# Performance work log

Hardware: AMD Instinct MI355X
Metric: run time of the kernel (lower is better)

The kernel has to match this reference:

```python
import jax, jax.numpy as jnp
import numpy as np

B, L, D, H = 2, 2048, 2048, 16
HD = D // H  # head_dim = 128
EPS = 1e-5


def setup_inputs() -> dict:
    key = jax.random.key(0)
    ks = jax.random.split(key, 5)
    return {
        "x": jax.random.normal(ks[0], (B, L, D), dtype=jnp.float32),
        "Wq": jax.random.normal(ks[1], (D, D), dtype=jnp.float32) * (D ** -0.5),
        "Wk": jax.random.normal(ks[2], (D, D), dtype=jnp.float32) * (D ** -0.5),
        "Wv": jax.random.normal(ks[3], (D, D), dtype=jnp.float32) * (D ** -0.5),
        "gamma_logit": jax.random.normal(ks[4], (H,), dtype=jnp.float32),
        "gn_weight": jnp.ones((D,), dtype=jnp.float32),
        "gn_bias": jnp.zeros((D,), dtype=jnp.float32),
    }


def reference(x, Wq, Wk, Wv, gamma_logit, gn_weight, gn_bias):
    scale = HD ** -0.5
    # projections (torch Linear: y = x @ W.T)
    Q = jnp.einsum('bld,ed->ble', x, Wq).reshape(B, L, H, HD).transpose(0, 2, 1, 3)
    K = jnp.einsum('bld,ed->ble', x, Wk).reshape(B, L, H, HD).transpose(0, 2, 1, 3)
    V = jnp.einsum('bld,ed->ble', x, Wv).reshape(B, L, H, HD).transpose(0, 2, 1, 3)
    # causal exponential decay matrix D[h,i,j] = gamma_h^(i-j), lower-triangular
    pos = jnp.arange(L)
    dist = jnp.abs(pos[None, :] - pos[:, None]).astype(jnp.float32)  # [L,L]
    gamma = jax.nn.sigmoid(gamma_logit)  # [H]
    Dmat = jnp.tril(gamma[:, None, None] ** dist[None, :, :])  # [H,L,L]
    # decayed linear attention (no softmax)
    attn = jnp.einsum('bhid,bhjd->bhij', Q, K) * scale * Dmat[None]
    out = jnp.einsum('bhij,bhje->bhie', attn, V)  # [B,H,L,HD]
    out = out.transpose(0, 2, 1, 3)  # [B,L,H,HD]
    # GroupNorm: channels=D, groups=H, spatial=L -> normalize per (b,h) over (L,HD)
    mean = out.mean(axis=(1, 3), keepdims=True)
    var = out.var(axis=(1, 3), keepdims=True)
    y = (out - mean) * jax.lax.rsqrt(var + EPS)
    y = y * gn_weight.reshape(1, 1, H, HD) + gn_bias.reshape(1, 1, H, HD)
    return y.reshape(B, L, D)
```

## Files before the change

kernel.cpp:

```cpp
#include <hip/hip_runtime.h>
#include <hip/hip_bf16.h>
#include <math.h>

#define B_  2
#define L_  2048
#define D_  2048
#define H_  16
#define HD_ 128
#define EPS_ 1e-5f

typedef __attribute__((ext_vector_type(8)))  short short8;
typedef __attribute__((ext_vector_type(4)))  float f32x4;
typedef __attribute__((ext_vector_type(16))) float f32x16;

static __device__ inline unsigned short bfb(float x) {
    __hip_bfloat16 h = __float2bfloat16(x);
    unsigned short s;
    __builtin_memcpy(&s, &h, 2);
    return s;
}
static __device__ inline unsigned pk2(float a, float b) {
    return (unsigned)bfb(a) | ((unsigned)bfb(b) << 16);
}

static __device__ __forceinline__ void gld_lds16(const void* g, void* l) {
    __builtin_amdgcn_global_load_lds(
        (const __attribute__((address_space(1))) unsigned int*)g,
        (__attribute__((address_space(3))) unsigned int*)l,
        16, 0, 0);
}

#define XN4 2097152
#define WN4 1048576
#define TOT4 (XN4 + 3 * WN4)

__global__ __launch_bounds__(256) void cast4_kernel(
    const float* __restrict__ x,  const float* __restrict__ Wq,
    const float* __restrict__ Wk, const float* __restrict__ Wv,
    __hip_bfloat16* __restrict__ dst)
{
    int i = blockIdx.x * 256 + threadIdx.x;
    const int st = gridDim.x * 256;
    for (; i < TOT4; i += st) {
        const float* s;
        int off;
        if (i < XN4)                { s = x;  off = i; }
        else if (i < XN4 + WN4)     { s = Wq; off = i - XN4; }
        else if (i < XN4 + 2 * WN4) { s = Wk; off = i - XN4 - WN4; }
        else                        { s = Wv; off = i - XN4 - 2 * WN4; }
        float4 v = ((const float4*)s)[off];
        uint2 r;
        r.x = pk2(v.x, v.y);
        r.y = pk2(v.z, v.w);
        ((uint2*)dst)[i] = r;
    }
}

__global__ __launch_bounds__(256) void proj_bf16(
    const __hip_bfloat16* __restrict__ X,
    const __hip_bfloat16* __restrict__ Wqb, const __hip_bfloat16* __restrict__ Wkb,
    const __hip_bfloat16* __restrict__ Wvb,
    __hip_bfloat16* __restrict__ Qo, __hip_bfloat16* __restrict__ Ko,
    __hip_bfloat16* __restrict__ Vt)
{
    const __hip_bfloat16* W = (blockIdx.z == 0) ? Wqb : (blockIdx.z == 1 ? Wkb : Wvb);
    __hip_bfloat16*       O = (blockIdx.z == 0) ? Qo  : (blockIdx.z == 1 ? Ko  : Vt);

    __shared__ __align__(16) char Al[128 * 64 * 2];
    __shared__ __align__(16) char Bl[128 * 64 * 2];

    const int t  = threadIdx.x;
    const int w  = t >> 6, l = t & 63;
    const int li = l & 15, hi4 = l >> 4;
    const int wr = w >> 1, wcn = w & 1;
    const int m0 = blockIdx.y * 128;
    const int n0 = blockIdx.x * 128;

    const int srow = l >> 3;
    const int scol = ((l & 7) ^ (l >> 3)) * 8;

    f32x4 acc[4][4];
    #pragma unroll
    for (int i = 0; i < 4; ++i)
        #pragma unroll
        for (int j = 0; j < 4; ++j)
            #pragma unroll
            for (int r = 0; r < 4; ++r) acc[i][j][r] = 0.f;

    for (int k0 = 0; k0 < D_; k0 += 64) {
        if (k0) __syncthreads();
        #pragma unroll
        for (int c = 0; c < 4; ++c) {
            const int chunk = w * 4 + c;
            const int row   = chunk * 8 + srow;
            gld_lds16(X + (size_t)(m0 + row) * D_ + k0 + scol, Al + chunk * 1024);
            gld_lds16(W + (size_t)(n0 + row) * D_ + k0 + scol, Bl + chunk * 1024);
        }
        __syncthreads();

        #pragma unroll
        for (int s = 0; s < 2; ++s) {
            const int cbA = (s * 64 + hi4 * 16) ^ ((li & 7) << 4);
            short8 af[4], bf[4];
            #pragma unroll
            for (int mi = 0; mi < 4; ++mi)
                af[mi] = *(const short8*)(Al + (wr * 64 + mi * 16 + li) * 128 + cbA);
            #pragma unroll
            for (int ni = 0; ni < 4; ++ni)
                bf[ni] = *(const short8*)(Bl + (wcn * 64 + ni * 16 + li) * 128 + cbA);
            #pragma unroll
            for (int mi = 0; mi < 4; ++mi)
                #pragma unroll
                for (int ni = 0; ni < 4; ++ni)
                    acc[mi][ni] = __builtin_amdgcn_mfma_f32_16x16x32_bf16(
                        af[mi], bf[ni], acc[mi][ni], 0, 0, 0);
        }
    }

    if (blockIdx.z == 2) {
        #pragma unroll
        for (int mi = 0; mi < 4; ++mi) {
            #pragma unroll
            for (int ni = 0; ni < 4; ++ni) {
                const int n     = n0 + wcn * 64 + ni * 16 + li;
                const int mbase = m0 + wr * 64 + mi * 16 + hi4 * 4;
                const int b = mbase >> 11, ml = mbase & (L_ - 1);
                uint2 w2;
                w2.x = pk2(acc[mi][ni][0], acc[mi][ni][1]);
                w2.y = pk2(acc[mi][ni][2], acc[mi][ni][3]);
                *(uint2*)&O[((size_t)b * (H_ * HD_) + n) * L_ + ml] = w2;
            }
        }
    } else {
        #pragma unroll
        for (int mi = 0; mi < 4; ++mi) {
            #pragma unroll
            for (int ni = 0; ni < 4; ++ni) {
                const int n  = n0 + wcn * 64 + ni * 16 + li;
                const int h  = n >> 7, hd = n & (HD_ - 1);
                #pragma unroll
                for (int r = 0; r < 4; ++r) {
                    const int m = m0 + wr * 64 + mi * 16 + hi4 * 4 + r;
                    const int b = m >> 11, ml = m & (L_ - 1);
                    O[((size_t)(b * H_ + h) * L_ + ml) * HD_ + hd] =
                        __float2bfloat16(acc[mi][ni][r]);
                }
            }
        }
    }
}

__global__ __launch_bounds__(256) void retn_kernel(
    const __hip_bfloat16* __restrict__ Qb, const __hip_bfloat16* __restrict__ Kb,
    const __hip_bfloat16* __restrict__ VT, const float* __restrict__ gl,
    float* __restrict__ out, float2* __restrict__ part)
{
    const int bid = blockIdx.x;
    const int mm  = bid >> 5;
    const int m   = (mm < 8) ? (15 - mm) : (mm - 8);
    const int bh  = bid & 31;
    const int b   = bh >> 4, h = bh & (H_ - 1);
    const int t   = threadIdx.x;
    const int w   = t >> 6, l = t & 63;
    const int li  = l & 31, hi = l >> 5;

    const float gamma = 1.f / (1.f + __expf(-gl[h]));
    const float lg2   = __log2f(gamma);
    const float scale = 0.08838834764831845f;

    __shared__ __align__(16) char Klds[32768];
    __shared__ __align__(16) char Vlds[32768];
    __shared__ float rs[4], rq[4];

    const size_t base = (size_t)bh * (L_ * HD_);
    const __hip_bfloat16* VTg = VT + (size_t)bh * (HD_ * L_);
    const int i0 = m * 128 + w * 32;

    short8 qf[8];
    {
        const __hip_bfloat16* qrow = Qb + base + (size_t)(i0 + li) * HD_;
        #pragma unroll
        for (int s = 0; s < 8; ++s)
            qf[s] = *(const short8*)(qrow + s * 16 + hi * 8);
    }

    float df[16];
    #pragma unroll
    for (int r = 0; r < 16; ++r) {
        const int jl = (r & 3) + 8 * (r >> 2) + 4 * hi;
        df[r] = exp2f(lg2 * (float)(li - jl));
    }

    f32x16 acc[4];
    #pragma unroll
    for (int c = 0; c < 4; ++c)
        #pragma unroll
        for (int r = 0; r < 16; ++r) acc[c][r] = 0.f;

    const int srow4 = l >> 4;
    const int sslot = l & 15;

    for (int gj = 0; gj <= m * 128; gj += 128) {
        __syncthreads();
        #pragma unroll
        for (int cc = 0; cc < 8; ++cc) {
            const int c  = w * 8 + cc;
            const int r  = c * 4 + srow4;
            const int sc = ((sslot ^ (r & 15)) * 8);
            gld_lds16(Kb + base + (size_t)(gj + r) * HD_ + sc, Klds + c * 1024);
            gld_lds16(VTg + (size_t)r * L_ + gj + sc,          Vlds + c * 1024);
        }
        __syncthreads();

        const int tmax = ((i0 - gj) >> 5) < 3 ? ((i0 - gj) >> 5) : 3;
        for (int jt = 0; jt <= tmax; ++jt) {
            const int j0 = gj + jt * 32;

            f32x16 c;
            #pragma unroll
            for (int r = 0; r < 16; ++r) c[r] = 0.f;
            #pragma unroll
            for (int s = 0; s < 8; ++s) {
                short8 kf = *(const short8*)(Klds + (jt * 32 + li) * 256 +
                                             (((s * 2 + hi) ^ (li & 15)) << 4));
                c = __builtin_amdgcn_mfma_f32_32x32x16_bf16(kf, qf[s], c, 0, 0, 0);
            }

            float p[16];
            const float bt = exp2f(lg2 * (float)(i0 - j0)) * scale;
            if (j0 == i0) {
                #pragma unroll
                for (int r = 0; r < 16; ++r) {
                    const int jl = (r & 3) + 8 * (r >> 2) + 4 * hi;
                    p[r] = (jl <= li) ? c[r] * (df[r] * bt) : 0.f;
                }
            } else {
                #pragma unroll
                for (int r = 0; r < 16; ++r) p[r] = c[r] * (df[r] * bt);
            }

            #pragma unroll
            for (int sl = 0; sl < 2; ++sl) {
                const int o = sl * 8;
                unsigned pk01 = pk2(p[o + 0], p[o + 1]);
                unsigned pk23 = pk2(p[o + 2], p[o + 3]);
                unsigned pk45 = pk2(p[o + 4], p[o + 5]);
                unsigned pk67 = pk2(p[o + 6], p[o + 7]);
                unsigned x01 = (unsigned)__shfl_xor((int)pk01, 32);
                unsigned x23 = (unsigned)__shfl_xor((int)pk23, 32);
                unsigned x45 = (unsigned)__shfl_xor((int)pk45, 32);
                unsigned x67 = (unsigned)__shfl_xor((int)pk67, 32);
                union { short8 v; unsigned u[4]; } pf;
                pf.u[0] = hi ? x45 : pk01;
                pf.u[1] = hi ? x67 : pk23;
                pf.u[2] = hi ? pk45 : x01;
                pf.u[3] = hi ? pk67 : x23;
                #pragma unroll
                for (int cch = 0; cch < 4; ++cch) {
                    short8 vf = *(const short8*)(Vlds + (cch * 32 + li) * 256 +
                                 (((jt * 4 + sl * 2 + hi) ^ (li & 15)) << 4));
                    acc[cch] = __builtin_amdgcn_mfma_f32_32x32x16_bf16(
                        pf.v, vf, acc[cch], 0, 0, 0);
                }
            }
        }
    }

    float s = 0.f, sq = 0.f;
    #pragma unroll
    for (int cch = 0; cch < 4; ++cch) {
        #pragma unroll
        for (int r = 0; r < 16; ++r) {
            const int row = (r & 3) + 8 * (r >> 2) + 4 * hi;
            const float v = acc[cch][r];
            out[(size_t)(b * L_ + i0 + row) * D_ + h * HD_ + cch * 32 + li] = v;
            s += v; sq += v * v;
        }
    }

    #pragma unroll
    for (int off = 32; off > 0; off >>= 1) {
        s  += __shfl_down(s, off);
        sq += __shfl_down(sq, off);
    }
    if (l == 0) { rs[w] = s; rq[w] = sq; }
    __syncthreads();
    if (t == 0)
        part[bh * 16 + m] = make_float2(rs[0] + rs[1] + rs[2] + rs[3],
                                        rq[0] + rq[1] + rq[2] + rq[3]);
}

__global__ __launch_bounds__(256) void gn_apply(
    float* __restrict__ out, const float2* __restrict__ part,
    const float* __restrict__ gw, const float* __restrict__ gb)
{
    const int bh = blockIdx.x, sl = blockIdx.y;
    const int b = bh >> 4, h = bh & (H_ - 1);
    const int t = threadIdx.x;

    float S = 0.f, SQ = 0.f;
    #pragma unroll
    for (int i = 0; i < 16; ++i) {
        float2 p = part[bh * 16 + i];
        S += p.x; SQ += p.y;
    }
    const float inv  = 1.f / (float)(L_ * HD_);
    const float mean = S * inv;
    float var = SQ * inv - mean * mean;
    if (var < 0.f) var = 0.f;
    const float rstd = rsqrtf(var + EPS_);

    #pragma unroll
    for (int it = 0; it < 4; ++it) {
        const int n  = it * 256 + t;
        const int ll = n >> 5, d4 = n & 31;
        const size_t idx = (size_t)(b * L_ + sl * 32 + ll) * D_ + h * HD_ + d4 * 4;
        float4 v = *(const float4*)&out[idx];
        const float4 w4 = *(const float4*)&gw[h * HD_ + d4 * 4];
        const float4 b4 = *(const float4*)&gb[h * HD_ + d4 * 4];
        v.x = (v.x - mean) * rstd * w4.x + b4.x;
        v.y = (v.y - mean) * rstd * w4.y + b4.y;
        v.z = (v.z - mean) * rstd * w4.z + b4.z;
        v.w = (v.w - mean) * rstd * w4.w + b4.w;
        *(float4*)&out[idx] = v;
    }
}

extern "C" void kernel_launch(void* const* d_in, const int* in_sizes, int n_in,
                              void* d_out, int out_size, void* d_ws, size_t ws_size,
                              hipStream_t stream) {
    const float* x  = (const float*)d_in[0];
    const float* Wq = (const float*)d_in[1];
    const float* Wk = (const float*)d_in[2];
    const float* Wv = (const float*)d_in[3];
    const float* gl = (const float*)d_in[4];
    const float* gw = (const float*)d_in[5];
    const float* gb = (const float*)d_in[6];
    float* out = (float*)d_out;

    __hip_bfloat16* ws = (__hip_bfloat16*)d_ws;
    __hip_bfloat16* xb  = ws;
    __hip_bfloat16* Wqb = xb  + 8388608;
    __hip_bfloat16* Wkb = Wqb + 4194304;
    __hip_bfloat16* Wvb = Wkb + 4194304;
    __hip_bfloat16* Qbf = Wvb + 4194304;
    __hip_bfloat16* Kbf = Qbf + 8388608;
    __hip_bfloat16* VTb = Kbf + 8388608;
    float2* part = (float2*)(VTb + 8388608);

    cast4_kernel<<<2048, 256, 0, stream>>>(x, Wq, Wk, Wv, xb);

    dim3 pgrid(D_ / 128, (B_ * L_) / 128, 3);
    proj_bf16<<<pgrid, 256, 0, stream>>>(xb, Wqb, Wkb, Wvb, Qbf, Kbf, VTb);

    retn_kernel<<<dim3(512), 256, 0, stream>>>(Qbf, Kbf, VTb, gl, out, part);

    gn_apply<<<dim3(32, 64), 256, 0, stream>>>(out, part, gw, gb);
}
```

Measured before the change: 220.3 us.

## Use chunked recurrent state for retention instead of full quadratic causal loop

Switches the decayed linear attention to a chunkwise form. The projection kernel also writes a transposed K. A new kernel computes a decay-weighted K^T V state for each 128-token chunk, and a scan kernel accumulates these states across chunks with gamma^128 decay. The retention kernel then applies the carried-in state with one MFMA pass and processes only its own diagonal chunk, which removes the quadratic loop over all earlier key blocks. In exchange it adds two kernel launches, an extra K write, and bf16 storage of the states. The path is only enabled when the workspace exceeds a size threshold.

```diff
diff --git a/kernel.cpp b/kernel.cpp
--- a/kernel.cpp
+++ b/kernel.cpp
@@ -21,6 +21,12 @@
 }
 static __device__ inline unsigned pk2(float a, float b) {
     return (unsigned)bfb(a) | ((unsigned)bfb(b) << 16);
+}
+static __device__ inline float bf2f(unsigned short u) {
+    unsigned v = ((unsigned)u) << 16;
+    float f;
+    __builtin_memcpy(&f, &v, 4);
+    return f;
 }
 
 static __device__ __forceinline__ void gld_lds16(const void* g, void* l) {
@@ -61,7 +67,7 @@
     const __hip_bfloat16* __restrict__ Wqb, const __hip_bfloat16* __restrict__ Wkb,
     const __hip_bfloat16* __restrict__ Wvb,
     __hip_bfloat16* __restrict__ Qo, __hip_bfloat16* __restrict__ Ko,
-    __hip_bfloat16* __restrict__ Vt)
+    __hip_bfloat16* __restrict__ Vt, __hip_bfloat16* __restrict__ Kt)
 {
     const __hip_bfloat16* W = (blockIdx.z == 0) ? Wqb : (blockIdx.z == 1 ? Wkb : Wvb);
     __hip_bfloat16*       O = (blockIdx.z == 0) ? Qo  : (blockIdx.z == 1 ? Ko  : Vt);
@@ -147,17 +153,125 @@
                 }
             }
         }
+        if (blockIdx.z == 1 && Kt != nullptr) {
+            #pragma unroll
+            for (int mi = 0; mi < 4; ++mi) {
+                #pragma unroll
+                for (int ni = 0; ni < 4; ++ni) {
+                    const int n     = n0 + wcn * 64 + ni * 16 + li;
+                    const int mbase = m0 + wr * 64 + mi * 16 + hi4 * 4;
+                    const int b = mbase >> 11, ml = mbase & (L_ - 1);
+                    uint2 w2;
+                    w2.x = pk2(acc[mi][ni][0], acc[mi][ni][1]);
+                    w2.y = pk2(acc[mi][ni][2], acc[mi][ni][3]);
+                    *(uint2*)&Kt[((size_t)b * (H_ * HD_) + n) * L_ + ml] = w2;
+                }
+            }
+        }
+    }
+}
+
+__global__ __launch_bounds__(256) void state_part(
+    const __hip_bfloat16* __restrict__ KT, const __hip_bfloat16* __restrict__ VT,
+    const float* __restrict__ gl, __hip_bfloat16* __restrict__ SpT)
+{
+    const int bid = blockIdx.x;
+    const int bh  = bid & 31, c = bid >> 5;
+    const int h   = bh & (H_ - 1);
+    const int t   = threadIdx.x;
+    const int w   = t >> 6, l = t & 63;
+    const int li  = l & 31, hi = l >> 5;
+
+    const float gamma = 1.f / (1.f + __expf(-gl[h]));
+    const float lg2   = __log2f(gamma);
+
+    __shared__ __align__(16) char Kl[32768];
+    __shared__ __align__(16) char Vl[32768];
+
+    const __hip_bfloat16* KTg = KT + (size_t)bh * (HD_ * L_);
+    const __hip_bfloat16* VTg = VT + (size_t)bh * (HD_ * L_);
+    const int gj = c * 128;
+    const int srow4 = l >> 4, sslot = l & 15;
+
+    #pragma unroll
+    for (int cc = 0; cc < 8; ++cc) {
+        const int ch = w * 8 + cc;
+        const int r  = ch * 4 + srow4;
+        const int sc = ((sslot ^ (r & 15)) * 8);
+        gld_lds16(KTg + (size_t)r * L_ + gj + sc, Kl + ch * 1024);
+        gld_lds16(VTg + (size_t)r * L_ + gj + sc, Vl + ch * 1024);
+    }
+    __syncthreads();
+
+    f32x16 acc[4];
+    #pragma unroll
+    for (int cch = 0; cch < 4; ++cch)
+        #pragma unroll
+        for (int r = 0; r < 16; ++r) acc[cch][r] = 0.f;
+
+    #pragma unroll
+    for (int s = 0; s < 8; ++s) {
+        const int boff = ((s * 2 + hi) ^ (li & 15)) << 4;
+        short8 vraw = *(const short8*)(Vl + (w * 32 + li) * 256 + boff);
+        short8 af;
+        #pragma unroll
+        for (int e = 0; e < 8; ++e) {
+            const int jl = s * 16 + hi * 8 + e;
+            const float f = bf2f((unsigned short)vraw[e]) *
+                            exp2f(lg2 * (float)(127 - jl));
+            af[e] = (short)bfb(f);
+        }
+        #pragma unroll
+        for (int cch = 0; cch < 4; ++cch) {
+            short8 bf = *(const short8*)(Kl + (cch * 32 + li) * 256 + boff);
+            acc[cch] = __builtin_amdgcn_mfma_f32_32x32x16_bf16(af, bf, acc[cch], 0, 0, 0);
+        }
+    }
+
+    __hip_bfloat16* Sp = SpT + (size_t)(bh * 16 + c) * 16384;
+    #pragma unroll
+    for (int cch = 0; cch < 4; ++cch)
+        #pragma unroll
+        for (int r = 0; r < 16; ++r) {
+            const int d = w * 32 + (r & 3) + 8 * (r >> 2) + 4 * hi;
+            Sp[(size_t)d * 128 + cch * 32 + li] = __float2bfloat16(acc[cch][r]);
+        }
+}
+
+__global__ __launch_bounds__(256) void state_scan(
+    const __hip_bfloat16* __restrict__ SpT, __hip_bfloat16* __restrict__ SbT,
+    const float* __restrict__ gl)
+{
+    const int bh = blockIdx.x;
+    const int h  = bh & (H_ - 1);
+    const float gamma = 1.f / (1.f + __expf(-gl[h]));
+    const float g128  = exp2f(__log2f(gamma) * 128.f);
+    const int fid = blockIdx.y * 256 + threadIdx.x;
+
+    float a0 = 0.f, a1 = 0.f, a2 = 0.f, a3 = 0.f;
+    for (int c = 0; c < 16; ++c) {
+        const size_t off = (size_t)(bh * 16 + c) * 16384 + (size_t)fid * 4;
+        uint2 v = *(const uint2*)(SpT + off);
+        a0 = g128 * a0 + bf2f((unsigned short)(v.x & 0xffff));
+        a1 = g128 * a1 + bf2f((unsigned short)(v.x >> 16));
+        a2 = g128 * a2 + bf2f((unsigned short)(v.y & 0xffff));
+        a3 = g128 * a3 + bf2f((unsigned short)(v.y >> 16));
+        uint2 o;
+        o.x = pk2(a0, a1);
+        o.y = pk2(a2, a3);
+        *(uint2*)(SbT + off) = o;
     }
 }
 
 __global__ __launch_bounds__(256) void retn_kernel(
     const __hip_bfloat16* __restrict__ Qb, const __hip_bfloat16* __restrict__ Kb,
     const __hip_bfloat16* __restrict__ VT, const float* __restrict__ gl,
-    float* __restrict__ out, float2* __restrict__ part)
+    float* __restrict__ out, float2* __restrict__ part,
+    const __hip_bfloat16* __restrict__ SbT, int use_chunks)
 {
     const int bid = blockIdx.x;
     const int mm  = bid >> 5;
-    const int m   = (mm < 8) ? (15 - mm) : (mm - 8);
+    const int m   = use_chunks ? mm : ((mm < 8) ? (15 - mm) : (mm - 8));
     const int bh  = bid & 31;
     const int b   = bh >> 4, h = bh & (H_ - 1);
     const int t   = threadIdx.x;
@@ -200,7 +314,36 @@
     const int srow4 = l >> 4;
     const int sslot = l & 15;
 
-    for (int gj = 0; gj <= m * 128; gj += 128) {
+    if (use_chunks && m > 0) {
+        const __hip_bfloat16* Sg = SbT + (size_t)(bh * 16 + (m - 1)) * 16384;
+        #pragma unroll
+        for (int cc = 0; cc < 8; ++cc) {
+            const int ch = w * 8 + cc;
+            const int r  = ch * 4 + srow4;
+            const int sc = ((sslot ^ (r & 15)) * 8);
+            gld_lds16(Sg + (size_t)r * 128 + sc, Klds + ch * 1024);
+        }
+        __syncthreads();
+        #pragma unroll
+        for (int s = 0; s < 8; ++s) {
+            const int boff = ((s * 2 + hi) ^ (li & 15)) << 4;
+            #pragma unroll
+            for (int cch = 0; cch < 4; ++cch) {
+                short8 sf = *(const short8*)(Klds + (cch * 32 + li) * 256 + boff);
+                acc[cch] = __builtin_amdgcn_mfma_f32_32x32x16_bf16(
+                    qf[s], sf, acc[cch], 0, 0, 0);
+            }
+        }
+        #pragma unroll
+        for (int r = 0; r < 16; ++r) {
+            const int il = (r & 3) + 8 * (r >> 2) + 4 * hi + w * 32;
+            const float fr = exp2f(lg2 * (float)(il + 1)) * scale;
+            acc[0][r] *= fr; acc[1][r] *= fr; acc[2][r] *= fr; acc[3][r] *= fr;
+        }
+    }
+
+    const int gj0 = use_chunks ? m * 128 : 0;
+    for (int gj = gj0; gj <= m * 128; gj += 128) {
         __syncthreads();
         #pragma unroll
         for (int cc = 0; cc < 8; ++cc) {
@@ -347,13 +490,27 @@
     __hip_bfloat16* Kbf = Qbf + 8388608;
     __hip_bfloat16* VTb = Kbf + 8388608;
     float2* part = (float2*)(VTb + 8388608);
+    __hip_bfloat16* KTb = (__hip_bfloat16*)(part + 512);
+
+    __hip_bfloat16* SpT = xb;
+    __hip_bfloat16* SbT = Wqb;
+
+    const int use_chunks = (ws_size >= 109056000ULL) ? 1 : 0;
 
     cast4_kernel<<<2048, 256, 0, stream>>>(x, Wq, Wk, Wv, xb);
 
     dim3 pgrid(D_ / 128, (B_ * L_) / 128, 3);
-    proj_bf16<<<pgrid, 256, 0, stream>>>(xb, Wqb, Wkb, Wvb, Qbf, Kbf, VTb);
-
-    retn_kernel<<<dim3(512), 256, 0, stream>>>(Qbf, Kbf, VTb, gl, out, part);
+    proj_bf16<<<pgrid, 256, 0, stream>>>(xb, Wqb, Wkb, Wvb, Qbf, Kbf, VTb,
+                                         use_chunks ? KTb : nullptr);
+
+    if (use_chunks) {
+        state_part<<<dim3(512), 256, 0, stream>>>(KTb, VTb, gl, SpT);
+        state_scan<<<dim3(32, 16), 256, 0, stream>>>(SpT, SbT, gl);
+    }
+
+    retn_kernel<<<dim3(512), 256, 0, stream>>>(Qbf, Kbf, VTb, gl, out, part,
+                                               use_chunks ? SbT : nullptr,
+                                               use_chunks);
 
     gn_apply<<<dim3(32, 64), 256, 0, stream>>>(out, part, gw, gb);
 }
```

Measured after the change: 189.1 us. -14.1%, faster.
